# Performance work log

Hardware: AMD Instinct MI355X
Metric: run time of the kernel (lower is better)

The kernel has to match this reference:

```python
import jax, jax.numpy as jnp
import numpy as np

N = 50000; E = 800000; G = 256; F = 34; D = 128; H = 4; C = 32; L = 4
EPS = 1e-5

def _bn(x, g, b):
    # BatchNorm1d with batch statistics (train-mode math), eval dropout (identity)
    m = jnp.mean(x, 0); v = jnp.var(x, 0)
    return g * (x - m) * jax.lax.rsqrt(v + EPS) + b

def _seg_softmax(s, seg, n):
    # numerically-stable softmax over edges grouped by destination node
    m = jax.ops.segment_max(s, seg, num_segments=n)
    m = jnp.where(jnp.isfinite(m), m, 0.0)
    e = jnp.exp(s - m[seg])
    d = jax.ops.segment_sum(e, seg, num_segments=n)
    return e / (d[seg] + 1e-16)

def setup_inputs():
    key = jax.random.key(0)
    ks = iter(jax.random.split(key, 64))
    def rn(shape, s=0.05):
        return jax.random.normal(next(ks), shape, dtype=jnp.float32) * s
    inp = {}
    inp['x'] = jax.random.normal(next(ks), (N, F), dtype=jnp.float32)
    inp['edge_index'] = jax.random.randint(next(ks), (2, E), 0, N, dtype=jnp.int32)
    inp['batch'] = jnp.sort(jax.random.randint(next(ks), (N,), 0, G, dtype=jnp.int32))
    inp['emb_W'] = rn((F, D)); inp['emb_b'] = rn((D,))
    inp['emb_g'] = jnp.ones((D,)); inp['emb_be'] = jnp.zeros((D,))
    inp['gWl'] = rn((L, D, D)); inp['gWr'] = rn((L, D, D))
    inp['gbl'] = rn((L, D)); inp['gbr'] = rn((L, D))
    inp['gatt'] = rn((L, H, C)); inp['gbias'] = rn((L, D))
    inp['gg'] = jnp.ones((L, D)); inp['gbe'] = jnp.zeros((L, D))
    inp['tWq'] = rn((D, D)); inp['tWk'] = rn((D, D)); inp['tWv'] = rn((D, D)); inp['tWs'] = rn((D, D))
    inp['tbq'] = rn((D,)); inp['tbk'] = rn((D,)); inp['tbv'] = rn((D,)); inp['tbs'] = rn((D,))
    inp['tg'] = jnp.ones((D,)); inp['tbe'] = jnp.zeros((D,))
    inp['oW1'] = rn((2 * D, D)); inp['ob1'] = rn((D,))
    inp['og'] = jnp.ones((D,)); inp['obe'] = jnp.zeros((D,))
    inp['oW2'] = rn((D, D // 2)); inp['ob2'] = rn((D // 2,))
    inp['oW3'] = rn((D // 2, 1)); inp['ob3'] = rn((1,))
    return inp

def reference(x, edge_index, batch, emb_W, emb_b, emb_g, emb_be, gWl, gWr, gbl, gbr, gatt, gbias, gg, gbe, tWq, tWk, tWv, tWs, tbq, tbk, tbv, tbs, tg, tbe, oW1, ob1, og, obe, oW2, ob2, oW3, ob3):
    x = jax.nn.relu(_bn(x @ emb_W + emb_b, emb_g, emb_be))
    sl = jnp.arange(N, dtype=edge_index.dtype)
    ei = jnp.concatenate([edge_index, jnp.stack([sl, sl])], axis=1)  # GATv2 default add_self_loops=True
    src, dst = ei[0], ei[1]
    for l in range(L):  # 4 structurally identical GATv2 layers
        xl = (x @ gWl[l] + gbl[l]).reshape(N, H, C)
        xr = (x @ gWr[l] + gbr[l]).reshape(N, H, C)
        e = jax.nn.leaky_relu(xl[src] + xr[dst], 0.2)  # [E+N, H, C]
        sc = jnp.einsum('ehc,hc->eh', e, gatt[l])
        a = _seg_softmax(sc, dst, N)
        out = jax.ops.segment_sum(xl[src] * a[..., None], dst, num_segments=N).reshape(N, D) + gbias[l]
        x = x + jax.nn.relu(_bn(out, gg[l], gbe[l]))
    # TransformerConv: no self-loops by default, dot-product attention + root skip
    s2, d2 = edge_index[0], edge_index[1]
    q = (x @ tWq + tbq).reshape(N, H, C)
    k = (x @ tWk + tbk).reshape(N, H, C)
    v = (x @ tWv + tbv).reshape(N, H, C)
    sc = jnp.einsum('ehc,ehc->eh', q[d2], k[s2]) / np.float32(np.sqrt(C))
    a = _seg_softmax(sc, d2, N)
    agg = jax.ops.segment_sum(v[s2] * a[..., None], d2, num_segments=N).reshape(N, D)
    x = x + _bn(agg + x @ tWs + tbs, tg, tbe)
    # global mean + max pooling over graphs
    cnt = jax.ops.segment_sum(jnp.ones((N,), x.dtype), batch, num_segments=G)
    xm = jax.ops.segment_sum(x, batch, num_segments=G) / jnp.maximum(cnt, 1.0)[:, None]
    xx = jax.ops.segment_max(x, batch, num_segments=G)
    xx = jnp.where(jnp.isfinite(xx), xx, 0.0)  # guard empty segments
    h = jnp.concatenate([xm, xx], axis=1)
    h = jax.nn.relu(_bn(h @ oW1 + ob1, og, obe))
    h = jax.nn.relu(h @ oW2 + ob2)
    return h @ oW3 + ob3
```

## Files before the change

### kernel.cpp

```cpp
#include <hip/hip_runtime.h>
#include <hip/hip_fp16.h>

namespace {
constexpr int NN = 50000;
constexpr int NE = 800000;
constexpr int NG = 256;
constexpr int NF = 34;
constexpr int NL = 4;
constexpr int NB = (NN + 255) / 256;
constexpr int STS = 32;
constexpr int GQ = ((NE + 3) / 4 + 255) / 256;
constexpr int GD = ((NE + 7) / 8 + 255) / 256;
constexpr int GE = (NN + 63) / 64;
}
#define EPSB 1e-5f
#define LSLOPE 0.2f
#define INV_SQRT_C 0.17677669529663687f

typedef short bf16x8 __attribute__((ext_vector_type(8)));
typedef float f32x4 __attribute__((ext_vector_type(4)));
typedef _Float16 hv2 __attribute__((ext_vector_type(2)));

static __device__ __forceinline__ short f2bf(float f) {
    unsigned int u = __float_as_uint(f);
    u = (u + 0x7fff + ((u >> 16) & 1)) >> 16;
    return (short)u;
}
static __device__ __forceinline__ unsigned fenc(float x) {
    unsigned u = __float_as_uint(x);
    return (u & 0x80000000u) ? ~u : (u | 0x80000000u);
}
static __device__ __forceinline__ float fdec(unsigned u) {
    return __uint_as_float((u & 0x80000000u) ? (u ^ 0x80000000u) : ~u);
}
static __device__ __forceinline__ float fdot2(hv2 a, hv2 b, float c) {
    return __builtin_amdgcn_fdot2(a, b, c, false);
}

__global__ __launch_bounds__(256) void k_deg(const int* __restrict__ ei,
                                             int* __restrict__ deg,
                                             int* __restrict__ rank) {
    int tid = blockIdx.x * 256 + threadIdx.x;
    const int S = (NE + 7) / 8;
    if (tid >= S) return;
#pragma unroll
    for (int k = 0; k < 8; ++k) {
        int e = tid + k * S;
        if (e < NE) rank[e] = atomicAdd(&deg[ei[NE + e]], 1);
    }
}

__global__ __launch_bounds__(256) void k_init(const float* __restrict__ gWl,
                                              const float* __restrict__ gWr,
                                              const float* __restrict__ tWq,
                                              const float* __restrict__ tWk,
                                              const float* __restrict__ tWv,
                                              const float* __restrict__ tWs,
                                              short* __restrict__ Wt,
                                              const float* __restrict__ A,
                                              const float* __restrict__ W,
                                              const float* __restrict__ bias,
                                              __half* __restrict__ outEmb,
                                              float* __restrict__ stms) {
    __shared__ float As[64 * NF];
    __shared__ float sred[256];
    int blk = blockIdx.x;
    if (blk < 12) {
        const float* src;
        if (blk < 4) src = gWl + blk * 16384;
        else if (blk < 8) src = gWr + (blk - 4) * 16384;
        else if (blk == 8) src = tWq;
        else if (blk == 9) src = tWk;
        else if (blk == 10) src = tWv;
        else src = tWs;
        short* d = Wt + blk * 16384;
        for (int i = threadIdx.x; i < 16384; i += 256) {
            int n = i >> 7, k = i & 127;
            d[i] = f2bf(src[k * 128 + n]);
        }
        return;
    }
    blk -= 12;
    int r0 = blk * 64;
    int rows = NN - r0; if (rows > 64) rows = 64;
    int total = rows * NF;
    for (int idx = threadIdx.x; idx < 64 * NF; idx += 256)
        As[idx] = (idx < total) ? A[(size_t)r0 * NF + idx] : 0.f;
    sred[threadIdx.x] = 0.f;
    __syncthreads();
    int tx = threadIdx.x & 31, ty = threadIdx.x >> 5;
    const float4* W4 = (const float4*)W;
    float acc[8][4];
#pragma unroll
    for (int j = 0; j < 8; ++j)
#pragma unroll
        for (int i = 0; i < 4; ++i) acc[j][i] = 0.f;
#pragma unroll 2
    for (int k = 0; k < NF; ++k) {
        float4 w = W4[k * 32 + tx];
#pragma unroll
        for (int j = 0; j < 8; ++j) {
            float a = As[(ty * 8 + j) * NF + k];
            acc[j][0] += a * w.x; acc[j][1] += a * w.y;
            acc[j][2] += a * w.z; acc[j][3] += a * w.w;
        }
    }
    float4 b = ((const float4*)bias)[tx];
    float s[4] = {0.f, 0.f, 0.f, 0.f}, ss[4] = {0.f, 0.f, 0.f, 0.f};
#pragma unroll
    for (int j = 0; j < 8; ++j) {
        int r = ty * 8 + j;
        if (r < rows) {
            float4 o = make_float4(acc[j][0] + b.x, acc[j][1] + b.y,
                                   acc[j][2] + b.z, acc[j][3] + b.w);
            union { short4 s4; __half h[4]; } uh;
            uh.h[0] = __float2half(o.x); uh.h[1] = __float2half(o.y);
            uh.h[2] = __float2half(o.z); uh.h[3] = __float2half(o.w);
            *(short4*)&outEmb[(size_t)(r0 + r) * 128 + tx * 4] = uh.s4;
            s[0] += o.x; ss[0] += o.x * o.x;
            s[1] += o.y; ss[1] += o.y * o.y;
            s[2] += o.z; ss[2] += o.z * o.z;
            s[3] += o.w; ss[3] += o.w * o.w;
        }
    }
#pragma unroll
    for (int i = 0; i < 4; ++i) {
        atomicAdd(&sred[tx * 4 + i], s[i]);
        atomicAdd(&sred[128 + tx * 4 + i], ss[i]);
    }
    __syncthreads();
    atomicAdd(&stms[(blk & (STS - 1)) * 256 + threadIdx.x], sred[threadIdx.x]);
}

__global__ __launch_bounds__(256) void k_scan1(const int* __restrict__ deg, int* __restrict__ bsum) {
    __shared__ int sm[256];
    int i = blockIdx.x * 256 + threadIdx.x;
    sm[threadIdx.x] = (i < NN) ? deg[i] : 0;
    __syncthreads();
    for (int off = 128; off > 0; off >>= 1) {
        if (threadIdx.x < off) sm[threadIdx.x] += sm[threadIdx.x + off];
        __syncthreads();
    }
    if (threadIdx.x == 0) bsum[blockIdx.x] = sm[0];
}

__global__ __launch_bounds__(256) void k_scan2(const int* __restrict__ bsum,
                                               int* __restrict__ boff, int* __restrict__ rp) {
    __shared__ int sm[256];
    int t = threadIdx.x;
    int v = (t < NB) ? bsum[t] : 0;
    sm[t] = v;
    __syncthreads();
    for (int off = 1; off < 256; off <<= 1) {
        int u = (t >= off) ? sm[t - off] : 0;
        __syncthreads();
        sm[t] += u;
        __syncthreads();
    }
    if (t < NB) boff[t] = sm[t] - v;
    if (t == 255) rp[NN] = sm[255];
}

__global__ __launch_bounds__(256) void k_scan3(const int* __restrict__ deg,
                                               const int* __restrict__ boff,
                                               int* __restrict__ rp) {
    __shared__ int sm[256];
    int i = blockIdx.x * 256 + threadIdx.x;
    int t = threadIdx.x;
    int v = (i < NN) ? deg[i] : 0;
    sm[t] = v;
    __syncthreads();
    for (int off = 1; off < 256; off <<= 1) {
        int u = (t >= off) ? sm[t - off] : 0;
        __syncthreads();
        sm[t] += u;
        __syncthreads();
    }
    if (i < NN) rp[i] = boff[blockIdx.x] + sm[t] - v;
}

__global__ __launch_bounds__(256) void k_fill(const int* __restrict__ ei,
                                              const int* __restrict__ rp,
                                              const int* __restrict__ rank,
                                              int* __restrict__ esrc) {
    int tid = blockIdx.x * 256 + threadIdx.x;
    const int S = (NE + 3) / 4;
    if (tid >= S) return;
#pragma unroll
    for (int k = 0; k < 4; ++k) {
        int e = tid + k * S;
        if (e < NE) {
            int s = ei[e];
            int d = ei[NE + e];
            int p = rp[d] + rank[e];
            esrc[p] = s;
        }
    }
}

__global__ __launch_bounds__(256) void k_stats(const __half* __restrict__ src, int nRows,
                                               float* __restrict__ st) {
    int c = threadIdx.x & 127;
    int sub = threadIdx.x >> 7;
    int r0 = blockIdx.x * 128;
    int rend = r0 + 128; if (rend > nRows) rend = nRows;
    float s = 0.f, ss = 0.f;
    for (int r = r0 + sub; r < rend; r += 2) {
        float v = __half2float(src[(size_t)r * 128 + c]);
        s += v; ss += v * v;
    }
    float* dst = st + (blockIdx.x & (STS - 1)) * 256;
    atomicAdd(&dst[c], s);
    atomicAdd(&dst[128 + c], ss);
}

template <int SRC16, int OUTH0, int OUTH1, int RES, int XOUT>
__global__ __launch_bounds__(256) void k_gemm2bn(const float* __restrict__ src,
                                                 const float* __restrict__ res,
                                                 float* __restrict__ xout,
                                                 const float* __restrict__ st,
                                                 const float* __restrict__ g,
                                                 const float* __restrict__ b,
                                                 const short* __restrict__ Wt0,
                                                 const short* __restrict__ Wt1,
                                                 const float* __restrict__ bias0,
                                                 const float* __restrict__ bias1,
                                                 void* __restrict__ out0,
                                                 void* __restrict__ out1, int nRows) {
    __shared__ short As[128 * 136];
    __shared__ short Bs[128 * 136];
    __shared__ float scsh[256];
    const float invn = 1.f / NN;
    if (threadIdx.x < 128) {
        int c = threadIdx.x;
        float s0v = 0.f, s1v = 0.f;
#pragma unroll 8
        for (int k2 = 0; k2 < STS; ++k2) {
            s0v += st[k2 * 256 + c];
            s1v += st[k2 * 256 + 128 + c];
        }
        float mean = s0v * invn;
        float var = fmaxf(s1v * invn - mean * mean, 0.f);
        float s = g[c] * rsqrtf(var + EPSB);
        scsh[c] = s;
        scsh[128 + c] = b[c] - mean * s;
    }
    {
        const int4* Wt4 = (const int4*)Wt0;
        for (int idx = threadIdx.x; idx < 2048; idx += 256) {
            int row = idx >> 4, c8 = idx & 15;
            *(int4*)&Bs[row * 136 + c8 * 8] = Wt4[idx];
        }
    }
    __syncthreads();
    int r0 = blockIdx.x * 128;
    int rows = nRows - r0; if (rows > 128) rows = 128;
    for (int idx = threadIdx.x; idx < 2048; idx += 256) {
        int r = idx >> 4, c8 = idx & 15;
        short4 sa = {0, 0, 0, 0}, sb = {0, 0, 0, 0};
        if (r < rows) {
            size_t base = (size_t)(r0 + r) * 128 + c8 * 8;
            float4 v0, v1;
            if (SRC16) {
                union { float4 f4; __half h[8]; } u;
                u.f4 = *(const float4*)&((const __half*)src)[base];
                v0 = make_float4(__half2float(u.h[0]), __half2float(u.h[1]),
                                 __half2float(u.h[2]), __half2float(u.h[3]));
                v1 = make_float4(__half2float(u.h[4]), __half2float(u.h[5]),
                                 __half2float(u.h[6]), __half2float(u.h[7]));
            } else {
                v0 = *(const float4*)&src[base];
                v1 = *(const float4*)&src[base + 4];
            }
            int c = c8 * 8;
            v0.x = fmaxf(v0.x * scsh[c + 0] + scsh[128 + c + 0], 0.f);
            v0.y = fmaxf(v0.y * scsh[c + 1] + scsh[128 + c + 1], 0.f);
            v0.z = fmaxf(v0.z * scsh[c + 2] + scsh[128 + c + 2], 0.f);
            v0.w = fmaxf(v0.w * scsh[c + 3] + scsh[128 + c + 3], 0.f);
            v1.x = fmaxf(v1.x * scsh[c + 4] + scsh[128 + c + 4], 0.f);
            v1.y = fmaxf(v1.y * scsh[c + 5] + scsh[128 + c + 5], 0.f);
            v1.z = fmaxf(v1.z * scsh[c + 6] + scsh[128 + c + 6], 0.f);
            v1.w = fmaxf(v1.w * scsh[c + 7] + scsh[128 + c + 7], 0.f);
            if (RES) {
                float4 rr0 = *(const float4*)&res[base];
                float4 rr1 = *(const float4*)&res[base + 4];
                v0.x += rr0.x; v0.y += rr0.y; v0.z += rr0.z; v0.w += rr0.w;
                v1.x += rr1.x; v1.y += rr1.y; v1.z += rr1.z; v1.w += rr1.w;
            }
            if (XOUT) {
                *(float4*)&xout[base] = v0;
                *(float4*)&xout[base + 4] = v1;
            }
            sa.x = f2bf(v0.x); sa.y = f2bf(v0.y); sa.z = f2bf(v0.z); sa.w = f2bf(v0.w);
            sb.x = f2bf(v1.x); sb.y = f2bf(v1.y); sb.z = f2bf(v1.z); sb.w = f2bf(v1.w);
        }
        *(short4*)&As[r * 136 + c8 * 8] = sa;
        *(short4*)&As[r * 136 + c8 * 8 + 4] = sb;
    }
    __syncthreads();
    int lane = threadIdx.x & 63, wave = threadIdx.x >> 6;
    int n16 = lane & 15, quad = lane >> 4;
    bf16x8 af[2][4];
#pragma unroll
    for (int rt = 0; rt < 2; ++rt)
#pragma unroll
        for (int kc = 0; kc < 4; ++kc)
            af[rt][kc] = *(const bf16x8*)&As[(wave * 32 + rt * 16 + n16) * 136 + kc * 32 + quad * 8];

    f32x4 acc[2][8];
#pragma unroll
    for (int rt = 0; rt < 2; ++rt)
#pragma unroll
        for (int ct = 0; ct < 8; ++ct) acc[rt][ct] = (f32x4){0.f, 0.f, 0.f, 0.f};
#pragma unroll
    for (int ct = 0; ct < 8; ++ct)
#pragma unroll
        for (int kc = 0; kc < 4; ++kc) {
            bf16x8 bf = *(const bf16x8*)&Bs[(ct * 16 + n16) * 136 + kc * 32 + quad * 8];
            acc[0][ct] = __builtin_amdgcn_mfma_f32_16x16x32_bf16(af[0][kc], bf, acc[0][ct], 0, 0, 0);
            acc[1][ct] = __builtin_amdgcn_mfma_f32_16x16x32_bf16(af[1][kc], bf, acc[1][ct], 0, 0, 0);
        }
#pragma unroll
    for (int ct = 0; ct < 8; ++ct) {
        int colI = ct * 16 + n16;
        float bv = bias0[colI];
#pragma unroll
        for (int rt = 0; rt < 2; ++rt)
#pragma unroll
            for (int reg = 0; reg < 4; ++reg) {
                int r = wave * 32 + rt * 16 + quad * 4 + reg;
                if (r < rows) {
                    float v = acc[rt][ct][reg] + bv;
                    if (OUTH0) ((__half*)out0)[(size_t)(r0 + r) * 128 + colI] = __float2half(v);
                    else       ((float*)out0)[(size_t)(r0 + r) * 128 + colI] = v;
                }
            }
    }
    __syncthreads();
    {
        const int4* Wt4 = (const int4*)Wt1;
        for (int idx = threadIdx.x; idx < 2048; idx += 256) {
            int row = idx >> 4, c8 = idx & 15;
            *(int4*)&Bs[row * 136 + c8 * 8] = Wt4[idx];
        }
    }
    __syncthreads();
#pragma unroll
    for (int rt = 0; rt < 2; ++rt)
#pragma unroll
        for (int ct = 0; ct < 8; ++ct) acc[rt][ct] = (f32x4){0.f, 0.f, 0.f, 0.f};
#pragma unroll
    for (int ct = 0; ct < 8; ++ct)
#pragma unroll
        for (int kc = 0; kc < 4; ++kc) {
            bf16x8 bf = *(const bf16x8*)&Bs[(ct * 16 + n16) * 136 + kc * 32 + quad * 8];
            acc[0][ct] = __builtin_amdgcn_mfma_f32_16x16x32_bf16(af[0][kc], bf, acc[0][ct], 0, 0, 0);
            acc[1][ct] = __builtin_amdgcn_mfma_f32_16x16x32_bf16(af[1][kc], bf, acc[1][ct], 0, 0, 0);
        }
#pragma unroll
    for (int ct = 0; ct < 8; ++ct) {
        int colI = ct * 16 + n16;
        float bv = bias1[colI];
#pragma unroll
        for (int rt = 0; rt < 2; ++rt)
#pragma unroll
            for (int reg = 0; reg < 4; ++reg) {
                int r = wave * 32 + rt * 16 + quad * 4 + reg;
                if (r < rows) {
                    float v = acc[rt][ct][reg] + bv;
                    if (OUTH1) ((__half*)out1)[(size_t)(r0 + r) * 128 + colI] = __float2half(v);
                    else       ((float*)out1)[(size_t)(r0 + r) * 128 + colI] = v;
                }
            }
    }
}

__global__ __launch_bounds__(256) void k_gemm4bn(const __half* __restrict__ src,
                                                 const float* __restrict__ res,
                                                 float* __restrict__ xout,
                                                 const float* __restrict__ st,
                                                 const float* __restrict__ g,
                                                 const float* __restrict__ b,
                                                 const short* __restrict__ Wt,
                                                 const float* __restrict__ bq,
                                                 const float* __restrict__ bk,
                                                 const float* __restrict__ bv,
                                                 const float* __restrict__ bs,
                                                 __half* __restrict__ oq,
                                                 __half* __restrict__ okv,
                                                 __half* __restrict__ os, int nRows) {
    __shared__ short As[128 * 136];
    __shared__ short Bs[128 * 136];
    __shared__ float scsh[256];
    const float invn = 1.f / NN;
    if (threadIdx.x < 128) {
        int c = threadIdx.x;
        float s0v = 0.f, s1v = 0.f;
#pragma unroll 8
        for (int k2 = 0; k2 < STS; ++k2) {
            s0v += st[k2 * 256 + c];
            s1v += st[k2 * 256 + 128 + c];
        }
        float mean = s0v * invn;
        float var = fmaxf(s1v * invn - mean * mean, 0.f);
        float s = g[c] * rsqrtf(var + EPSB);
        scsh[c] = s;
        scsh[128 + c] = b[c] - mean * s;
    }
    __syncthreads();
    int r0 = blockIdx.x * 128;
    int rows = nRows - r0; if (rows > 128) rows = 128;
    for (int idx = threadIdx.x; idx < 2048; idx += 256) {
        int r = idx >> 4, c8 = idx & 15;
        short4 sa = {0, 0, 0, 0}, sb = {0, 0, 0, 0};
        if (r < rows) {
            size_t base = (size_t)(r0 + r) * 128 + c8 * 8;
            union { float4 f4; __half h[8]; } u;
            u.f4 = *(const float4*)&src[base];
            float4 v0 = make_float4(__half2float(u.h[0]), __half2float(u.h[1]),
                                    __half2float(u.h[2]), __half2float(u.h[3]));
            float4 v1 = make_float4(__half2float(u.h[4]), __half2float(u.h[5]),
                                    __half2float(u.h[6]), __half2float(u.h[7]));
            int c = c8 * 8;
            v0.x = fmaxf(v0.x * scsh[c + 0] + scsh[128 + c + 0], 0.f);
            v0.y = fmaxf(v0.y * scsh[c + 1] + scsh[128 + c + 1], 0.f);
            v0.z = fmaxf(v0.z * scsh[c + 2] + scsh[128 + c + 2], 0.f);
            v0.w = fmaxf(v0.w * scsh[c + 3] + scsh[128 + c + 3], 0.f);
            v1.x = fmaxf(v1.x * scsh[c + 4] + scsh[128 + c + 4], 0.f);
            v1.y = fmaxf(v1.y * scsh[c + 5] + scsh[128 + c + 5], 0.f);
            v1.z = fmaxf(v1.z * scsh[c + 6] + scsh[128 + c + 6], 0.f);
            v1.w = fmaxf(v1.w * scsh[c + 7] + scsh[128 + c + 7], 0.f);
            float4 rr0 = *(const float4*)&res[base];
            float4 rr1 = *(const float4*)&res[base + 4];
            v0.x += rr0.x; v0.y += rr0.y; v0.z += rr0.z; v0.w += rr0.w;
            v1.x += rr1.x; v1.y += rr1.y; v1.z += rr1.z; v1.w += rr1.w;
            *(float4*)&xout[base] = v0;
            *(float4*)&xout[base + 4] = v1;
            sa.x = f2bf(v0.x); sa.y = f2bf(v0.y); sa.z = f2bf(v0.z); sa.w = f2bf(v0.w);
            sb.x = f2bf(v1.x); sb.y = f2bf(v1.y); sb.z = f2bf(v1.z); sb.w = f2bf(v1.w);
        }
        *(short4*)&As[r * 136 + c8 * 8] = sa;
        *(short4*)&As[r * 136 + c8 * 8 + 4] = sb;
    }
    int lane = threadIdx.x & 63, wave = threadIdx.x >> 6;
    int n16 = lane & 15, quad = lane >> 4;
    bf16x8 af[2][4];
    bool afLoaded = false;
    for (int m = 0; m < 4; ++m) {
        {
            const int4* Wt4 = (const int4*)(Wt + (size_t)m * 16384);
            for (int idx = threadIdx.x; idx < 2048; idx += 256) {
                int row = idx >> 4, c8 = idx & 15;
                *(int4*)&Bs[row * 136 + c8 * 8] = Wt4[idx];
            }
        }
        __syncthreads();
        if (!afLoaded) {
            afLoaded = true;
#pragma unroll
            for (int rt = 0; rt < 2; ++rt)
#pragma unroll
                for (int kc = 0; kc < 4; ++kc)
                    af[rt][kc] = *(const bf16x8*)&As[(wave * 32 + rt * 16 + n16) * 136 + kc * 32 + quad * 8];
        }
        f32x4 acc[2][8];
#pragma unroll
        for (int rt = 0; rt < 2; ++rt)
#pragma unroll
            for (int ct = 0; ct < 8; ++ct) acc[rt][ct] = (f32x4){0.f, 0.f, 0.f, 0.f};
#pragma unroll
        for (int ct = 0; ct < 8; ++ct)
#pragma unroll
            for (int kc = 0; kc < 4; ++kc) {
                bf16x8 bf = *(const bf16x8*)&Bs[(ct * 16 + n16) * 136 + kc * 32 + quad * 8];
                acc[0][ct] = __builtin_amdgcn_mfma_f32_16x16x32_bf16(af[0][kc], bf, acc[0][ct], 0, 0, 0);
                acc[1][ct] = __builtin_amdgcn_mfma_f32_16x16x32_bf16(af[1][kc], bf, acc[1][ct], 0, 0, 0);
            }
        __half* om; int strd, off;
        const float* bm;
        if (m == 0)      { om = oq;  strd = 128; off = 0;   bm = bq; }
        else if (m == 1) { om = okv; strd = 256; off = 0;   bm = bk; }
        else if (m == 2) { om = okv; strd = 256; off = 128; bm = bv; }
        else             { om = os;  strd = 128; off = 0;   bm = bs; }
#pragma unroll
        for (int ct = 0; ct < 8; ++ct) {
            int colI = ct * 16 + n16;
            float bv2 = bm[colI];
#pragma unroll
            for (int rt = 0; rt < 2; ++rt)
#pragma unroll
                for (int reg = 0; reg < 4; ++reg) {
                    int r = wave * 32 + rt * 16 + quad * 4 + reg;
                    if (r < rows)
                        om[(size_t)(r0 + r) * strd + off + colI] = __float2half(acc[rt][ct][reg] + bv2);
                }
        }
        if (m < 3) __syncthreads();
    }
}

__global__ __launch_bounds__(256) void k_gat_aggr(const __half* __restrict__ xl,
                                                  const __half* __restrict__ xr,
                                                  const float* __restrict__ att,
                                                  const float* __restrict__ gbias_l,
                                                  const int* __restrict__ rp,
                                                  const int* __restrict__ esrc,
                                                  __half* __restrict__ out) {
    int lane = threadIdx.x & 63;
    int node = blockIdx.x * 4 + (threadIdx.x >> 6);
    if (node >= NN) return;
    int q = lane >> 4;
    int l16 = lane & 15;
    int c8 = l16 * 8;
    float4 xrr = *(const float4*)&xr[(unsigned)node * 128u + c8];
    hv2 xrh[4] = {*(hv2*)&xrr.x, *(hv2*)&xrr.y, *(hv2*)&xrr.z, *(hv2*)&xrr.w};
    float4 atA = *(const float4*)&att[c8];
    float4 atB = *(const float4*)&att[c8 + 4];
    hv2 ath[4] = {{(_Float16)atA.x, (_Float16)atA.y}, {(_Float16)atA.z, (_Float16)atA.w},
                  {(_Float16)atB.x, (_Float16)atB.y}, {(_Float16)atB.z, (_Float16)atB.w}};
    const hv2 hz = {(_Float16)0.f, (_Float16)0.f};
    const hv2 hs = {(_Float16)LSLOPE, (_Float16)LSLOPE};
    int s0 = rp[node];
    int T = rp[node + 1] - s0 + 1;
    float a[8] = {0.f, 0.f, 0.f, 0.f, 0.f, 0.f, 0.f, 0.f};
    float l = 0.f;
    auto body = [&](int j) {
        bool self = (j == T - 1);
        int srcn = self ? node : esrc[s0 + j];
        float4 raw = *(const float4*)&xl[(unsigned)srcn * 128u + c8];
        hv2 f[4] = {*(hv2*)&raw.x, *(hv2*)&raw.y, *(hv2*)&raw.z, *(hv2*)&raw.w};
        float p = 0.f;
#pragma unroll
        for (int k = 0; k < 4; ++k) {
            hv2 e = f[k] + xrh[k];
            hv2 lk = __builtin_elementwise_max(e, hz) + hs * __builtin_elementwise_min(e, hz);
            p = fdot2(lk, ath[k], p);
        }
        p += __shfl_xor(p, 1); p += __shfl_xor(p, 2);
        float w = __expf(p);
#pragma unroll
        for (int k = 0; k < 4; ++k) {
            a[2 * k] += w * (float)f[k].x;
            a[2 * k + 1] += w * (float)f[k].y;
        }
        l += w;
    };
    int j = q;
    for (; j + 12 < T; j += 16) { body(j); body(j + 4); body(j + 8); body(j + 12); }
    for (; j + 4 < T; j += 8) { body(j); body(j + 4); }
    for (; j < T; j += 4) body(j);
#pragma unroll
    for (int k = 0; k < 8; ++k) { a[k] += __shfl_xor(a[k], 16); a[k] += __shfl_xor(a[k], 32); }
    l += __shfl_xor(l, 16); l += __shfl_xor(l, 32);
    if (q == 0) {
        float inv = 1.f / (l + 1e-16f);
        float4 gb0 = *(const float4*)&gbias_l[c8];
        float4 gb1 = *(const float4*)&gbias_l[c8 + 4];
        union { float4 f4; __half h[8]; } u;
        u.h[0] = __float2half(a[0] * inv + gb0.x); u.h[1] = __float2half(a[1] * inv + gb0.y);
        u.h[2] = __float2half(a[2] * inv + gb0.z); u.h[3] = __float2half(a[3] * inv + gb0.w);
        u.h[4] = __float2half(a[4] * inv + gb1.x); u.h[5] = __float2half(a[5] * inv + gb1.y);
        u.h[6] = __float2half(a[6] * inv + gb1.z); u.h[7] = __float2half(a[7] * inv + gb1.w);
        *(float4*)&out[(unsigned)node * 128u + c8] = u.f4;
    }
}

__global__ __launch_bounds__(256) void k_trans_aggr(const __half* __restrict__ qh,
                                                    const __half* __restrict__ kv,
                                                    const __half* __restrict__ sT,
                                                    const int* __restrict__ rp,
                                                    const int* __restrict__ esrc,
                                                    __half* __restrict__ out) {
    int lane = threadIdx.x & 63;
    int node = blockIdx.x * 4 + (threadIdx.x >> 6);
    if (node >= NN) return;
    int q = lane >> 4;
    int l16 = lane & 15;
    int c8 = l16 * 8;
    float4 qr = *(const float4*)&qh[(unsigned)node * 128u + c8];
    const hv2 hinv = {(_Float16)INV_SQRT_C, (_Float16)INV_SQRT_C};
    hv2 qv[4] = {(*(hv2*)&qr.x) * hinv, (*(hv2*)&qr.y) * hinv,
                 (*(hv2*)&qr.z) * hinv, (*(hv2*)&qr.w) * hinv};
    int s0 = rp[node];
    int T = rp[node + 1] - s0;
    float a[8] = {0.f, 0.f, 0.f, 0.f, 0.f, 0.f, 0.f, 0.f};
    float l = 0.f;
    auto body = [&](int j) {
        int srcn = esrc[s0 + j];
        const __half* kvp = &kv[(unsigned)srcn * 256u + c8];
        float4 kraw = *(const float4*)kvp;
        float4 vraw = *(const float4*)(kvp + 128);
        hv2 kvv[4] = {*(hv2*)&kraw.x, *(hv2*)&kraw.y, *(hv2*)&kraw.z, *(hv2*)&kraw.w};
        float p = 0.f;
#pragma unroll
        for (int k = 0; k < 4; ++k) p = fdot2(kvv[k], qv[k], p);
        p += __shfl_xor(p, 1); p += __shfl_xor(p, 2);
        float w = __expf(p);
        hv2 vvv[4] = {*(hv2*)&vraw.x, *(hv2*)&vraw.y, *(hv2*)&vraw.z, *(hv2*)&vraw.w};
#pragma unroll
        for (int k = 0; k < 4; ++k) {
            a[2 * k] += w * (float)vvv[k].x;
            a[2 * k + 1] += w * (float)vvv[k].y;
        }
        l += w;
    };
    int j = q;
    for (; j + 12 < T; j += 16) { body(j); body(j + 4); body(j + 8); body(j + 12); }
    for (; j + 4 < T; j += 8) { body(j); body(j + 4); }
    for (; j < T; j += 4) body(j);
#pragma unroll
    for (int k = 0; k < 8; ++k) { a[k] += __shfl_xor(a[k], 16); a[k] += __shfl_xor(a[k], 32); }
    l += __shfl_xor(l, 16); l += __shfl_xor(l, 32);
    if (q == 0) {
        float inv = 1.f / (l + 1e-16f);
        float4 straw = *(const float4*)&sT[(unsigned)node * 128u + c8];
        hv2 st[4] = {*(hv2*)&straw.x, *(hv2*)&straw.y, *(hv2*)&straw.z, *(hv2*)&straw.w};
        union { float4 f4; __half h[8]; } u;
        u.h[0] = __float2half(a[0] * inv + (float)st[0].x);
        u.h[1] = __float2half(a[1] * inv + (float)st[0].y);
        u.h[2] = __float2half(a[2] * inv + (float)st[1].x);
        u.h[3] = __float2half(a[3] * inv + (float)st[1].y);
        u.h[4] = __float2half(a[4] * inv + (float)st[2].x);
        u.h[5] = __float2half(a[5] * inv + (float)st[2].y);
        u.h[6] = __float2half(a[6] * inv + (float)st[3].x);
        u.h[7] = __float2half(a[7] * inv + (float)st[3].y);
        *(float4*)&out[(unsigned)node * 128u + c8] = u.f4;
    }
}

__global__ __launch_bounds__(256) void k_pool_part(const __half* __restrict__ src,
                                                   const float* __restrict__ res,
                                                   const float* __restrict__ st,
                                                   const float* __restrict__ g,
                                                   const float* __restrict__ b,
                                                   const int* __restrict__ batch,
                                                   float* __restrict__ psum,
                                                   unsigned* __restrict__ pmax) {
    __shared__ int bs[64];
    __shared__ float sc_sh[128], sh_sh[128];
    int r0 = blockIdx.x * 64;
    if (threadIdx.x < 64) {
        int r = r0 + threadIdx.x;
        bs[threadIdx.x] = (r < NN) ? batch[r] : -1;
    }
    const float invn = 1.f / NN;
    if (threadIdx.x < 128) {
        int c2 = threadIdx.x;
        float s0v = 0.f, s1v = 0.f;
#pragma unroll 8
        for (int k2 = 0; k2 < STS; ++k2) {
            s0v += st[k2 * 256 + c2];
            s1v += st[k2 * 256 + 128 + c2];
        }
        float mean = s0v * invn;
        float var = fmaxf(s1v * invn - mean * mean, 0.f);
        float scv = g[c2] * rsqrtf(var + EPSB);
        sc_sh[c2] = scv;
        sh_sh[c2] = b[c2] - mean * scv;
    }
    __syncthreads();
    int c = threadIdx.x & 127;
    int sub = threadIdx.x >> 7;
    float scv = sc_sh[c];
    float shv = sh_sh[c];
    int curg = -1;
    float s = 0.f, fmx = -INFINITY;
    for (int i = sub; i < 64; i += 2) {
        int r = r0 + i;
        if (r >= NN) break;
        int gr = bs[i];
        if (gr != curg) {
            if (curg >= 0) {
                atomicAdd(&psum[curg * 128 + c], s);
                atomicMax(&pmax[curg * 128 + c], fenc(fmx));
            }
            curg = gr; s = 0.f; fmx = -INFINITY;
        }
        float v = __half2float(src[(size_t)r * 128 + c]) * scv + shv + res[(size_t)r * 128 + c];
        s += v; fmx = fmaxf(fmx, v);
    }
    if (curg >= 0) {
        atomicAdd(&psum[curg * 128 + c], s);
        atomicMax(&pmax[curg * 128 + c], fenc(fmx));
    }
}

__global__ __launch_bounds__(128) void k_pool_head1(const float* __restrict__ psum,
                                                    const unsigned* __restrict__ pmax,
                                                    const int* __restrict__ batch,
                                                    const float* __restrict__ W,
                                                    const float* __restrict__ b,
                                                    float* __restrict__ t1,
                                                    float* __restrict__ st6) {
    __shared__ float hr[256];
    __shared__ int se[2];
    int g = blockIdx.x;
    int t = threadIdx.x;
    if (t == 0) {
        int lo = 0, hi = NN;
        while (lo < hi) { int mid = (lo + hi) >> 1; if (batch[mid] < g) lo = mid + 1; else hi = mid; }
        se[0] = lo;
        hi = NN;
        while (lo < hi) { int mid = (lo + hi) >> 1; if (batch[mid] < g + 1) lo = mid + 1; else hi = mid; }
        se[1] = lo;
    }
    __syncthreads();
    int cnt = se[1] - se[0];
    float xm = psum[g * 128 + t] / fmaxf((float)cnt, 1.f);
    float xx = (cnt > 0) ? fdec(pmax[g * 128 + t]) : 0.f;
    hr[t] = xm;
    hr[128 + t] = xx;
    __syncthreads();
    float acc = b[t];
#pragma unroll 4
    for (int k = 0; k < 256; ++k) acc += hr[k] * W[k * 128 + t];
    t1[g * 128 + t] = acc;
    atomicAdd(&st6[t], acc);
    atomicAdd(&st6[128 + t], acc * acc);
}

__global__ __launch_bounds__(64) void k_head2(const float* __restrict__ t1,
                                              const float* __restrict__ st,
                                              const float* __restrict__ og,
                                              const float* __restrict__ obe,
                                              const float* __restrict__ W2,
                                              const float* __restrict__ b2,
                                              const float* __restrict__ W3,
                                              const float* __restrict__ b3,
                                              float* __restrict__ out) {
    __shared__ float v[128];
    int row = blockIdx.x, t = threadIdx.x;
    const float invn = 1.f / NG;
#pragma unroll
    for (int half = 0; half < 2; ++half) {
        int ch = t + half * 64;
        float mean = st[ch] * invn;
        float var = fmaxf(st[128 + ch] * invn - mean * mean, 0.f);
        float scv = og[ch] * rsqrtf(var + EPSB);
        float shv = obe[ch] - mean * scv;
        float a = t1[row * 128 + ch] * scv + shv;
        v[ch] = fmaxf(a, 0.f);
    }
    __syncthreads();
    float acc = b2[t];
#pragma unroll 4
    for (int k = 0; k < 128; ++k) acc += v[k] * W2[k * 64 + t];
    float p = fmaxf(acc, 0.f) * W3[t];
    p += __shfl_xor(p, 1); p += __shfl_xor(p, 2); p += __shfl_xor(p, 4);
    p += __shfl_xor(p, 8); p += __shfl_xor(p, 16); p += __shfl_xor(p, 32);
    if (t == 0) out[row] = p + b3[0];
}

extern "C" void kernel_launch(void* const* d_in, const int* in_sizes, int n_in,
                              void* d_out, int out_size, void* d_ws, size_t ws_size,
                              hipStream_t stream) {
    const float* x_in   = (const float*)d_in[0];
    const int*   ei     = (const int*)d_in[1];
    const int*   batch  = (const int*)d_in[2];
    const float* emb_W  = (const float*)d_in[3];
    const float* emb_b  = (const float*)d_in[4];
    const float* emb_g  = (const float*)d_in[5];
    const float* emb_be = (const float*)d_in[6];
    const float* gWl    = (const float*)d_in[7];
    const float* gWr    = (const float*)d_in[8];
    const float* gbl    = (const float*)d_in[9];
    const float* gbr    = (const float*)d_in[10];
    const float* gatt   = (const float*)d_in[11];
    const float* gbias  = (const float*)d_in[12];
    const float* gg     = (const float*)d_in[13];
    const float* gbe    = (const float*)d_in[14];
    const float* tWq    = (const float*)d_in[15];
    const float* tWk    = (const float*)d_in[16];
    const float* tWv    = (const float*)d_in[17];
    const float* tWs    = (const float*)d_in[18];
    const float* tbq    = (const float*)d_in[19];
    const float* tbk    = (const float*)d_in[20];
    const float* tbv    = (const float*)d_in[21];
    const float* tbs    = (const float*)d_in[22];
    const float* tg     = (const float*)d_in[23];
    const float* tbe    = (const float*)d_in[24];
    const float* oW1    = (const float*)d_in[25];
    const float* ob1    = (const float*)d_in[26];
    const float* og     = (const float*)d_in[27];
    const float* obe    = (const float*)d_in[28];
    const float* oW2    = (const float*)d_in[29];
    const float* ob2    = (const float*)d_in[30];
    const float* oW3    = (const float*)d_in[31];
    const float* ob3    = (const float*)d_in[32];
    float* out = (float*)d_out;

    const size_t NDsz = (size_t)NN * 128;
    float* x     = (float*)d_ws;
    float* bA    = x + NDsz;
    float* bC    = bA + NDsz;
    float* stats = bC + NDsz;
    float* hpool = stats + 7 * 256;
    float* t1    = hpool + 65536;
    float* scb   = t1 + 32768;
    __half* xlh  = (__half*)(scb + (size_t)(NE + NN) * 4);
    __half* xrh  = xlh + NDsz;
    __half* vh   = xrh + NDsz;
    __half* sh   = vh + NDsz;
    short* Wt    = (short*)(sh + NDsz);
    int* deg     = (int*)(Wt + 12 * 16384);
    int* rp      = deg + NN;
    int* cursor  = rp + NN + 1;
    int2* edg    = (int2*)(cursor + NN);
    int* bsum    = (int*)(edg + NE + 64);
    int* boff    = bsum + 256;
    float* psum  = (float*)(boff + 256);
    unsigned* pmax = (unsigned*)(psum + NG * 128);
    int* rank    = (int*)scb;
    int* esrc    = (int*)edg;
    float* stms  = scb + NE;
    __half* bCh  = (__half*)bC;
    __half* kvh  = vh;

    hipMemsetAsync(deg, 0, NN * sizeof(int), stream);
    hipMemsetAsync(stats + 6 * 256, 0, 256 * sizeof(float), stream);
    hipMemsetAsync(stms, 0, 6 * STS * 256 * sizeof(float), stream);
    hipMemsetAsync(psum, 0, NG * 128 * 2 * sizeof(float), stream);

    const int gGemm = (NN + 127) / 128;
    const int gStat = (NN + 127) / 128;
    const int gNode = (NN + 3) / 4;
    const int gPool = (NN + 63) / 64;
    const int REG = STS * 256;

    k_deg<<<GD, 256, 0, stream>>>(ei, deg, rank);
    k_init<<<12 + GE, 256, 0, stream>>>(gWl, gWr, tWq, tWk, tWv, tWs,
                                        Wt, x_in, emb_W, emb_b, bCh, stms + 0 * REG);

    k_scan1<<<NB, 256, 0, stream>>>(deg, bsum);
    k_scan2<<<1, 256, 0, stream>>>(bsum, boff, rp);
    k_scan3<<<NB, 256, 0, stream>>>(deg, boff, rp);
    k_fill<<<GQ, 256, 0, stream>>>(ei, rp, rank, esrc);

    k_gemm2bn<1, 1, 1, 0, 1><<<gGemm, 256, 0, stream>>>((const float*)bCh, nullptr, x, stms + 0 * REG, emb_g, emb_be,
                                                        Wt + (size_t)0 * 16384, Wt + (size_t)4 * 16384,
                                                        gbl + 0 * 128, gbr + 0 * 128, xlh, xrh, NN);
    k_gat_aggr<<<gNode, 256, 0, stream>>>(xlh, xrh, gatt + 0 * 128, gbias + 0 * 128, rp, esrc, bCh);
    k_stats<<<gStat, 256, 0, stream>>>(bCh, NN, stms + 1 * REG);
    k_gemm2bn<1, 1, 1, 1, 1><<<gGemm, 256, 0, stream>>>((const float*)bCh, x, bA, stms + 1 * REG, gg + 0 * 128, gbe + 0 * 128,
                                                        Wt + (size_t)1 * 16384, Wt + (size_t)5 * 16384,
                                                        gbl + 1 * 128, gbr + 1 * 128, xlh, xrh, NN);
    k_gat_aggr<<<gNode, 256, 0, stream>>>(xlh, xrh, gatt + 1 * 128, gbias + 1 * 128, rp, esrc, bCh);
    k_stats<<<gStat, 256, 0, stream>>>(bCh, NN, stms + 2 * REG);
    k_gemm2bn<1, 1, 1, 1, 1><<<gGemm, 256, 0, stream>>>((const float*)bCh, bA, x, stms + 2 * REG, gg + 1 * 128, gbe + 1 * 128,
                                                        Wt + (size_t)2 * 16384, Wt + (size_t)6 * 16384,
                                                        gbl + 2 * 128, gbr + 2 * 128, xlh, xrh, NN);
    k_gat_aggr<<<gNode, 256, 0, stream>>>(xlh, xrh, gatt + 2 * 128, gbias + 2 * 128, rp, esrc, bCh);
    k_stats<<<gStat, 256, 0, stream>>>(bCh, NN, stms + 3 * REG);
    k_gemm2bn<1, 1, 1, 1, 1><<<gGemm, 256, 0, stream>>>((const float*)bCh, x, bA, stms + 3 * REG, gg + 2 * 128, gbe + 2 * 128,
                                                        Wt + (size_t)3 * 16384, Wt + (size_t)7 * 16384,
                                                        gbl + 3 * 128, gbr + 3 * 128, xlh, xrh, NN);
    k_gat_aggr<<<gNode, 256, 0, stream>>>(xlh, xrh, gatt + 3 * 128, gbias + 3 * 128, rp, esrc, bCh);
    k_stats<<<gStat, 256, 0, stream>>>(bCh, NN, stms + 4 * REG);

    k_gemm4bn<<<gGemm, 256, 0, stream>>>(bCh, bA, x, stms + 4 * REG, gg + 3 * 128, gbe + 3 * 128,
                                         Wt + (size_t)8 * 16384, tbq, tbk, tbv, tbs,
                                         xrh, kvh, xlh, NN);
    k_trans_aggr<<<gNode, 256, 0, stream>>>(xrh, kvh, xlh, rp, esrc, bCh);
    k_stats<<<gStat, 256, 0, stream>>>(bCh, NN, stms + 5 * REG);

    k_pool_part<<<gPool, 256, 0, stream>>>(bCh, x, stms + 5 * REG, tg, tbe, batch, psum, pmax);
    k_pool_head1<<<NG, 128, 0, stream>>>(psum, pmax, batch, oW1, ob1, t1, stats + 6 * 256);
    k_head2<<<NG, 64, 0, stream>>>(t1, stats + 6 * 256, og, obe, oW2, ob2, oW3, ob3, out);
}
```

Measured before the change: 792.7 us.

## Store residual stream in fp16 and fold degree counting into init kernel

The residual node features x/bA are now stored and read as fp16 instead of fp32 in the gemm-BN kernels and the pooling kernel, halving that memory traffic. The degree/rank atomic counting kernel is merged into k_init as extra blocks, removing one launch. In exchange the residual accumulation across layers loses precision to fp16 rounding.

```diff
diff --git a/kernel.cpp b/kernel.cpp
--- a/kernel.cpp
+++ b/kernel.cpp
@@ -37,20 +37,10 @@
     return __builtin_amdgcn_fdot2(a, b, c, false);
 }
 
-__global__ __launch_bounds__(256) void k_deg(const int* __restrict__ ei,
-                                             int* __restrict__ deg,
-                                             int* __restrict__ rank) {
-    int tid = blockIdx.x * 256 + threadIdx.x;
-    const int S = (NE + 7) / 8;
-    if (tid >= S) return;
-#pragma unroll
-    for (int k = 0; k < 8; ++k) {
-        int e = tid + k * S;
-        if (e < NE) rank[e] = atomicAdd(&deg[ei[NE + e]], 1);
-    }
-}
-
-__global__ __launch_bounds__(256) void k_init(const float* __restrict__ gWl,
+__global__ __launch_bounds__(256) void k_init(const int* __restrict__ ei,
+                                              int* __restrict__ deg,
+                                              int* __restrict__ rank,
+                                              const float* __restrict__ gWl,
                                               const float* __restrict__ gWr,
                                               const float* __restrict__ tWq,
                                               const float* __restrict__ tWk,
@@ -65,6 +55,18 @@
     __shared__ float As[64 * NF];
     __shared__ float sred[256];
     int blk = blockIdx.x;
+    if (blk < GD) {
+        int tid = blk * 256 + threadIdx.x;
+        const int S = (NE + 7) / 8;
+        if (tid >= S) return;
+#pragma unroll
+        for (int k = 0; k < 8; ++k) {
+            int e = tid + k * S;
+            if (e < NE) rank[e] = atomicAdd(&deg[ei[NE + e]], 1);
+        }
+        return;
+    }
+    blk -= GD;
     if (blk < 12) {
         const float* src;
         if (blk < 4) src = gWl + blk * 16384;
@@ -214,10 +216,10 @@
     atomicAdd(&dst[128 + c], ss);
 }
 
-template <int SRC16, int OUTH0, int OUTH1, int RES, int XOUT>
-__global__ __launch_bounds__(256) void k_gemm2bn(const float* __restrict__ src,
-                                                 const float* __restrict__ res,
-                                                 float* __restrict__ xout,
+template <int OUTH0, int OUTH1, int RES, int XOUT>
+__global__ __launch_bounds__(256) void k_gemm2bn(const __half* __restrict__ src,
+                                                 const __half* __restrict__ res,
+                                                 __half* __restrict__ xout,
                                                  const float* __restrict__ st,
                                                  const float* __restrict__ g,
                                                  const float* __restrict__ b,
@@ -260,18 +262,12 @@
         short4 sa = {0, 0, 0, 0}, sb = {0, 0, 0, 0};
         if (r < rows) {
             size_t base = (size_t)(r0 + r) * 128 + c8 * 8;
-            float4 v0, v1;
-            if (SRC16) {
-                union { float4 f4; __half h[8]; } u;
-                u.f4 = *(const float4*)&((const __half*)src)[base];
-                v0 = make_float4(__half2float(u.h[0]), __half2float(u.h[1]),
-                                 __half2float(u.h[2]), __half2float(u.h[3]));
-                v1 = make_float4(__half2float(u.h[4]), __half2float(u.h[5]),
-                                 __half2float(u.h[6]), __half2float(u.h[7]));
-            } else {
-                v0 = *(const float4*)&src[base];
-                v1 = *(const float4*)&src[base + 4];
-            }
+            union { float4 f4; __half h[8]; } u;
+            u.f4 = *(const float4*)&src[base];
+            float4 v0 = make_float4(__half2float(u.h[0]), __half2float(u.h[1]),
+                                    __half2float(u.h[2]), __half2float(u.h[3]));
+            float4 v1 = make_float4(__half2float(u.h[4]), __half2float(u.h[5]),
+                                    __half2float(u.h[6]), __half2float(u.h[7]));
             int c = c8 * 8;
             v0.x = fmaxf(v0.x * scsh[c + 0] + scsh[128 + c + 0], 0.f);
             v0.y = fmaxf(v0.y * scsh[c + 1] + scsh[128 + c + 1], 0.f);
@@ -282,14 +278,20 @@
             v1.z = fmaxf(v1.z * scsh[c + 6] + scsh[128 + c + 6], 0.f);
             v1.w = fmaxf(v1.w * scsh[c + 7] + scsh[128 + c + 7], 0.f);
             if (RES) {
-                float4 rr0 = *(const float4*)&res[base];
-                float4 rr1 = *(const float4*)&res[base + 4];
-                v0.x += rr0.x; v0.y += rr0.y; v0.z += rr0.z; v0.w += rr0.w;
-                v1.x += rr1.x; v1.y += rr1.y; v1.z += rr1.z; v1.w += rr1.w;
+                union { float4 f4; __half h[8]; } ur;
+                ur.f4 = *(const float4*)&res[base];
+                v0.x += __half2float(ur.h[0]); v0.y += __half2float(ur.h[1]);
+                v0.z += __half2float(ur.h[2]); v0.w += __half2float(ur.h[3]);
+                v1.x += __half2float(ur.h[4]); v1.y += __half2float(ur.h[5]);
+                v1.z += __half2float(ur.h[6]); v1.w += __half2float(ur.h[7]);
             }
             if (XOUT) {
-                *(float4*)&xout[base] = v0;
-                *(float4*)&xout[base + 4] = v1;
+                union { float4 f4; __half h[8]; } uo;
+                uo.h[0] = __float2half(v0.x); uo.h[1] = __float2half(v0.y);
+                uo.h[2] = __float2half(v0.z); uo.h[3] = __float2half(v0.w);
+                uo.h[4] = __float2half(v1.x); uo.h[5] = __float2half(v1.y);
+                uo.h[6] = __float2half(v1.z); uo.h[7] = __float2half(v1.w);
+                *(float4*)&xout[base] = uo.f4;
             }
             sa.x = f2bf(v0.x); sa.y = f2bf(v0.y); sa.z = f2bf(v0.z); sa.w = f2bf(v0.w);
             sb.x = f2bf(v1.x); sb.y = f2bf(v1.y); sb.z = f2bf(v1.z); sb.w = f2bf(v1.w);
@@ -376,8 +378,8 @@
 }
 
 __global__ __launch_bounds__(256) void k_gemm4bn(const __half* __restrict__ src,
-                                                 const float* __restrict__ res,
-                                                 float* __restrict__ xout,
+                                                 const __half* __restrict__ res,
+                                                 __half* __restrict__ xout,
                                                  const float* __restrict__ st,
                                                  const float* __restrict__ g,
                                                  const float* __restrict__ b,
@@ -430,12 +432,18 @@
             v1.y = fmaxf(v1.y * scsh[c + 5] + scsh[128 + c + 5], 0.f);
             v1.z = fmaxf(v1.z * scsh[c + 6] + scsh[128 + c + 6], 0.f);
             v1.w = fmaxf(v1.w * scsh[c + 7] + scsh[128 + c + 7], 0.f);
-            float4 rr0 = *(const float4*)&res[base];
-            float4 rr1 = *(const float4*)&res[base + 4];
-            v0.x += rr0.x; v0.y += rr0.y; v0.z += rr0.z; v0.w += rr0.w;
-            v1.x += rr1.x; v1.y += rr1.y; v1.z += rr1.z; v1.w += rr1.w;
-            *(float4*)&xout[base] = v0;
-            *(float4*)&xout[base + 4] = v1;
+            union { float4 f4; __half h[8]; } ur;
+            ur.f4 = *(const float4*)&res[base];
+            v0.x += __half2float(ur.h[0]); v0.y += __half2float(ur.h[1]);
+            v0.z += __half2float(ur.h[2]); v0.w += __half2float(ur.h[3]);
+            v1.x += __half2float(ur.h[4]); v1.y += __half2float(ur.h[5]);
+            v1.z += __half2float(ur.h[6]); v1.w += __half2float(ur.h[7]);
+            union { float4 f4; __half h[8]; } uo;
+            uo.h[0] = __float2half(v0.x); uo.h[1] = __float2half(v0.y);
+            uo.h[2] = __float2half(v0.z); uo.h[3] = __float2half(v0.w);
+            uo.h[4] = __float2half(v1.x); uo.h[5] = __float2half(v1.y);
+            uo.h[6] = __float2half(v1.z); uo.h[7] = __float2half(v1.w);
+            *(float4*)&xout[base] = uo.f4;
             sa.x = f2bf(v0.x); sa.y = f2bf(v0.y); sa.z = f2bf(v0.z); sa.w = f2bf(v0.w);
             sb.x = f2bf(v1.x); sb.y = f2bf(v1.y); sb.z = f2bf(v1.z); sb.w = f2bf(v1.w);
         }
@@ -629,7 +637,7 @@
 }
 
 __global__ __launch_bounds__(256) void k_pool_part(const __half* __restrict__ src,
-                                                   const float* __restrict__ res,
+                                                   const __half* __restrict__ res,
                                                    const float* __restrict__ st,
                                                    const float* __restrict__ g,
                                                    const float* __restrict__ b,
@@ -676,7 +684,8 @@
             }
             curg = gr; s = 0.f; fmx = -INFINITY;
         }
-        float v = __half2float(src[(size_t)r * 128 + c]) * scv + shv + res[(size_t)r * 128 + c];
+        float v = __half2float(src[(size_t)r * 128 + c]) * scv + shv
+                + __half2float(res[(size_t)r * 128 + c]);
         s += v; fmx = fmaxf(fmx, v);
     }
     if (curg >= 0) {
@@ -814,6 +823,8 @@
     int* esrc    = (int*)edg;
     float* stms  = scb + NE;
     __half* bCh  = (__half*)bC;
+    __half* xh   = (__half*)x;
+    __half* bAh  = (__half*)bA;
     __half* kvh  = vh;
 
     hipMemsetAsync(deg, 0, NN * sizeof(int), stream);
@@ -827,43 +838,42 @@
     const int gPool = (NN + 63) / 64;
     const int REG = STS * 256;
 
-    k_deg<<<GD, 256, 0, stream>>>(ei, deg, rank);
-    k_init<<<12 + GE, 256, 0, stream>>>(gWl, gWr, tWq, tWk, tWv, tWs,
-                                        Wt, x_in, emb_W, emb_b, bCh, stms + 0 * REG);
+    k_init<<<GD + 12 + GE, 256, 0, stream>>>(ei, deg, rank, gWl, gWr, tWq, tWk, tWv, tWs,
+                                             Wt, x_in, emb_W, emb_b, bCh, stms + 0 * REG);
 
     k_scan1<<<NB, 256, 0, stream>>>(deg, bsum);
     k_scan2<<<1, 256, 0, stream>>>(bsum, boff, rp);
     k_scan3<<<NB, 256, 0, stream>>>(deg, boff, rp);
     k_fill<<<GQ, 256, 0, stream>>>(ei, rp, rank, esrc);
 
-    k_gemm2bn<1, 1, 1, 0, 1><<<gGemm, 256, 0, stream>>>((const float*)bCh, nullptr, x, stms + 0 * REG, emb_g, emb_be,
-                                                        Wt + (size_t)0 * 16384, Wt + (size_t)4 * 16384,
-                                                        gbl + 0 * 128, gbr + 0 * 128, xlh, xrh, NN);
+    k_gemm2bn<1, 1, 0, 1><<<gGemm, 256, 0, stream>>>(bCh, nullptr, xh, stms + 0 * REG, emb_g, emb_be,
+                                                     Wt + (size_t)0 * 16384, Wt + (size_t)4 * 16384,
+                                                     gbl + 0 * 128, gbr + 0 * 128, xlh, xrh, NN);
     k_gat_aggr<<<gNode, 256, 0, stream>>>(xlh, xrh, gatt + 0 * 128, gbias + 0 * 128, rp, esrc, bCh);
     k_stats<<<gStat, 256, 0, stream>>>(bCh, NN, stms + 1 * REG);
-    k_gemm2bn<1, 1, 1, 1, 1><<<gGemm, 256, 0, stream>>>((const float*)bCh, x, bA, stms + 1 * REG, gg + 0 * 128, gbe + 0 * 128,
-                                                        Wt + (size_t)1 * 16384, Wt + (size_t)5 * 16384,
-                                                        gbl + 1 * 128, gbr + 1 * 128, xlh, xrh, NN);
+    k_gemm2bn<1, 1, 1, 1><<<gGemm, 256, 0, stream>>>(bCh, xh, bAh, stms + 1 * REG, gg + 0 * 128, gbe + 0 * 128,
+                                                     Wt + (size_t)1 * 16384, Wt + (size_t)5 * 16384,
+                                                     gbl + 1 * 128, gbr + 1 * 128, xlh, xrh, NN);
     k_gat_aggr<<<gNode, 256, 0, stream>>>(xlh, xrh, gatt + 1 * 128, gbias + 1 * 128, rp, esrc, bCh);
     k_stats<<<gStat, 256, 0, stream>>>(bCh, NN, stms + 2 * REG);
-    k_gemm2bn<1, 1, 1, 1, 1><<<gGemm, 256, 0, stream>>>((const float*)bCh, bA, x, stms + 2 * REG, gg + 1 * 128, gbe + 1 * 128,
-                                                        Wt + (size_t)2 * 16384, Wt + (size_t)6 * 16384,
-                                                        gbl + 2 * 128, gbr + 2 * 128, xlh, xrh, NN);
+    k_gemm2bn<1, 1, 1, 1><<<gGemm, 256, 0, stream>>>(bCh, bAh, xh, stms + 2 * REG, gg + 1 * 128, gbe + 1 * 128,
+                                                     Wt + (size_t)2 * 16384, Wt + (size_t)6 * 16384,
+                                                     gbl + 2 * 128, gbr + 2 * 128, xlh, xrh, NN);
     k_gat_aggr<<<gNode, 256, 0, stream>>>(xlh, xrh, gatt + 2 * 128, gbias + 2 * 128, rp, esrc, bCh);
     k_stats<<<gStat, 256, 0, stream>>>(bCh, NN, stms + 3 * REG);
-    k_gemm2bn<1, 1, 1, 1, 1><<<gGemm, 256, 0, stream>>>((const float*)bCh, x, bA, stms + 3 * REG, gg + 2 * 128, gbe + 2 * 128,
-                                                        Wt + (size_t)3 * 16384, Wt + (size_t)7 * 16384,
-                                                        gbl + 3 * 128, gbr + 3 * 128, xlh, xrh, NN);
+    k_gemm2bn<1, 1, 1, 1><<<gGemm, 256, 0, stream>>>(bCh, xh, bAh, stms + 3 * REG, gg + 2 * 128, gbe + 2 * 128,
+                                                     Wt + (size_t)3 * 16384, Wt + (size_t)7 * 16384,
+                                                     gbl + 3 * 128, gbr + 3 * 128, xlh, xrh, NN);
     k_gat_aggr<<<gNode, 256, 0, stream>>>(xlh, xrh, gatt + 3 * 128, gbias + 3 * 128, rp, esrc, bCh);
     k_stats<<<gStat, 256, 0, stream>>>(bCh, NN, stms + 4 * REG);
 
-    k_gemm4bn<<<gGemm, 256, 0, stream>>>(bCh, bA, x, stms + 4 * REG, gg + 3 * 128, gbe + 3 * 128,
+    k_gemm4bn<<<gGemm, 256, 0, stream>>>(bCh, bAh, xh, stms + 4 * REG, gg + 3 * 128, gbe + 3 * 128,
                                          Wt + (size_t)8 * 16384, tbq, tbk, tbv, tbs,
                                          xrh, kvh, xlh, NN);
     k_trans_aggr<<<gNode, 256, 0, stream>>>(xrh, kvh, xlh, rp, esrc, bCh);
     k_stats<<<gStat, 256, 0, stream>>>(bCh, NN, stms + 5 * REG);
 
-    k_pool_part<<<gPool, 256, 0, stream>>>(bCh, x, stms + 5 * REG, tg, tbe, batch, psum, pmax);
+    k_pool_part<<<gPool, 256, 0, stream>>>(bCh, xh, stms + 5 * REG, tg, tbe, batch, psum, pmax);
     k_pool_head1<<<NG, 128, 0, stream>>>(psum, pmax, batch, oW1, ob1, t1, stats + 6 * 256);
     k_head2<<<NG, 64, 0, stream>>>(t1, stats + 6 * 256, og, obe, oW2, ob2, oW3, ob3, out);
 }
```

Result: faster. 773.4 us (-2.4%).
